# Performance work log

Hardware: AMD Instinct MI355X
Metric: run time of the kernel (lower is better)

The kernel has to match this reference:

```python
import jax, jax.numpy as jnp
import numpy as np

V = 512          # num vertices
F = 64           # pair-feature dim (gpnn_channels in)
C = 64           # gpnn_channels out
E = 8192         # num edges (avg degree 16)


def setup_inputs() -> dict:
    key = jax.random.key(0)
    k1, k2, k3, k4 = jax.random.split(key, 4)
    alpha = jax.random.normal(k1, (V * V, F), dtype=jnp.float32)          # pair features, row v*V+w
    edge_index = jax.random.randint(k2, (2, E), 0, V)                      # COO [src; dst]
    # GPNNEdgeConv.nn = MLP([F, C, C], act='relu')  (norm treated as identity / eval stats)
    w1 = jax.random.normal(k3, (F, C), dtype=jnp.float32) * (1.0 / np.sqrt(F))
    b1 = jnp.zeros((C,), dtype=jnp.float32)
    w2 = jax.random.normal(k4, (C, C), dtype=jnp.float32) * (1.0 / np.sqrt(C))
    b2 = jnp.zeros((C,), dtype=jnp.float32)
    eps = jnp.asarray(0.0, dtype=jnp.float32)                              # train_eps parameter
    return {"alpha": alpha, "edge_index": edge_index,
            "w1": w1, "b1": b1, "w2": w2, "b2": b2, "eps": eps}


def reference(alpha, edge_index, w1, b1, w2, b2, eps):
    # Dense 0/1 adjacency adj_t: adj[v, j] = 1 iff edge j -> v (dst-indexed, as spmm(adj_t, .)).
    adj = jnp.zeros((V, V), dtype=alpha.dtype).at[edge_index[1], edge_index[0]].set(1.0)
    a3 = alpha.reshape(V, V, F)  # a3[v, j] = alpha[v*V + j]
    # message_and_aggregate: out[v*V+w] = row v of spmm(adj_t, A_{v,w}),
    # where A_{v,w}[j] = alpha[v*V+j] + alpha[w*V+j]  (sum aggregation)
    #   = sum_j adj[v,j] * (a3[v,j] + a3[w,j]) = S[v] + T[v,w]
    S = jnp.einsum('vj,vjf->vf', adj, a3)    # [V, F]
    T = jnp.einsum('vj,wjf->vwf', adj, a3)   # [V, V, F]
    out = (S[:, None, :] + T).reshape(V * V, F)
    # GINConv residual: out + (1 + eps) * x_r, then MLP (Linear-ReLU-Linear)
    out = out + (1.0 + eps) * alpha
    h = jax.nn.relu(out @ w1 + b1)
    return h @ w2 + b2
```

## Files before the change

kernel.cpp:

```cpp
#include <hip/hip_runtime.h>
#include <hip/hip_bf16.h>

#define NV 512
#define NF 64

typedef __attribute__((ext_vector_type(8))) short bf16x8;
typedef __attribute__((ext_vector_type(4))) float f32x4;

union BF8 { bf16x8 v; unsigned u[4]; };

__device__ __forceinline__ unsigned short f2bf(float x) {
    unsigned u = __float_as_uint(x);
    unsigned r = (u + 0x7fffu + ((u >> 16) & 1u)) >> 16;
    return (unsigned short)r;
}

__device__ __forceinline__ unsigned awt_addr(int f, int jbyte) {
    return (unsigned)((f * 1024 + jbyte) ^ (((f ^ (f >> 3)) & 7) << 4));
}
__device__ __forceinline__ unsigned wt_addr(int m, int n, int kbyte) {
    return (unsigned)(m * 8192 + ((n * 128 + kbyte) ^ (((n ^ (n >> 3)) & 7) << 4)));
}

__global__ void k_zero(unsigned int* mask) {
    mask[blockIdx.x * 256 + threadIdx.x] = 0u;
}

__global__ void k_edges(const int* __restrict__ ei, int E, unsigned int* __restrict__ mask) {
    int e = blockIdx.x * 256 + threadIdx.x;
    if (e < E) {
        int s = ei[e];
        int d = ei[E + e];
        atomicOr(&mask[d * 16 + (s >> 5)], 1u << (s & 31));
    }
}

__global__ void k_S(const unsigned int* __restrict__ mask, const float* __restrict__ alpha,
                    float* __restrict__ S) {
    int v = blockIdx.x;
    int f = threadIdx.x;
    float acc = 0.f;
    for (int wd = 0; wd < 16; ++wd) {
        unsigned int bits = mask[v * 16 + wd];
        while (bits) {
            int b = __ffs(bits) - 1;
            bits &= bits - 1;
            int j = wd * 32 + b;
            acc += alpha[((size_t)v * NV + j) * NF + f];
        }
    }
    S[v * NF + f] = acc;
}

#define SCR_OFF 65536

__global__ __launch_bounds__(512, 4) void k_main(
    const float* __restrict__ alpha, const float* __restrict__ w1, const float* __restrict__ b1,
    const float* __restrict__ w2, const float* __restrict__ b2, const float* __restrict__ eps_p,
    const unsigned int* __restrict__ mask, const float* __restrict__ S,
    float* __restrict__ out)
{
    extern __shared__ char smem[];

    const int w    = blockIdx.x;
    const int t    = threadIdx.x;
    const int lane = t & 63;
    const int wid  = t >> 6;
    const int nlo  = lane & 15;
    const int g    = lane >> 4;

    {
        const float* src = alpha + (size_t)w * (NV * NF);
#pragma unroll
        for (int i = 0; i < 2; ++i) {
            int task = i * 512 + t;
            int jb = task >> 4;
            int fq = task & 15;
            unsigned ua[4][4];
#pragma unroll
            for (int h = 0; h < 4; ++h) {
                f32x4 r0 = *(const f32x4*)(src + (size_t)(jb * 8 + 2 * h) * NF + fq * 4);
                f32x4 r1 = *(const f32x4*)(src + (size_t)(jb * 8 + 2 * h + 1) * NF + fq * 4);
#pragma unroll
                for (int c = 0; c < 4; ++c)
                    ua[c][h] = (unsigned)f2bf(r0[c]) | ((unsigned)f2bf(r1[c]) << 16);
            }
#pragma unroll
            for (int c = 0; c < 4; ++c) {
                BF8 p;
                p.u[0] = ua[c][0]; p.u[1] = ua[c][1]; p.u[2] = ua[c][2]; p.u[3] = ua[c][3];
                *(bf16x8*)(smem + awt_addr(fq * 4 + c, jb * 16)) = p.v;
            }
        }
    }

    const int mbase = wid * 64;
    unsigned qm[4][4];
#pragma unroll
    for (int mi = 0; mi < 4; ++mi) {
        const uint4 q = *(const uint4*)(mask + (size_t)(mbase + mi * 16 + nlo) * 16 + g * 4);
        qm[mi][0] = q.x; qm[mi][1] = q.y; qm[mi][2] = q.z; qm[mi][3] = q.w;
    }

    __syncthreads();

    f32x4 acc[4][4];
#pragma unroll
    for (int mi = 0; mi < 4; ++mi)
#pragma unroll
        for (int nt = 0; nt < 4; ++nt)
            acc[mi][nt] = (f32x4){0.f, 0.f, 0.f, 0.f};

#pragma unroll
    for (int kq = 0; kq < 4; ++kq)
#pragma unroll
        for (int kr = 0; kr < 4; ++kr) {
            const int kk = kq * 4 + kr;
            const int srcl = kq * 16 + nlo;
            BF8 afr[4];
#pragma unroll
            for (int mi = 0; mi < 4; ++mi) {
                unsigned word = (unsigned)__shfl((int)qm[mi][kr], srcl);
                unsigned byteb = (word >> (g * 8)) & 0xFFu;
#pragma unroll
                for (int h = 0; h < 4; ++h) {
                    unsigned b0 = (byteb >> (2 * h)) & 1u;
                    unsigned b1 = (byteb >> (2 * h + 1)) & 1u;
                    afr[mi].u[h] = (b0 ? 0x3F80u : 0u) | (b1 ? 0x3F800000u : 0u);
                }
            }
#pragma unroll
            for (int nt = 0; nt < 4; ++nt) {
                bf16x8 bfr = *(const bf16x8*)(smem + awt_addr(nt * 16 + nlo, kk * 64 + g * 16));
#pragma unroll
                for (int mi = 0; mi < 4; ++mi)
                    acc[mi][nt] = __builtin_amdgcn_mfma_f32_16x16x32_bf16(afr[mi].v, bfr, acc[mi][nt], 0, 0, 0);
            }
        }

    __syncthreads();

    if (t < 256) {
        int m  = t >> 7;
        int sub = t & 127;
        int jb = sub >> 4;
        int fq = sub & 15;
        const float* wsrc = m ? w2 : w1;
        unsigned ua[4][4];
#pragma unroll
        for (int h = 0; h < 4; ++h) {
            f32x4 r0 = *(const f32x4*)(wsrc + (size_t)(jb * 8 + 2 * h) * NF + fq * 4);
            f32x4 r1 = *(const f32x4*)(wsrc + (size_t)(jb * 8 + 2 * h + 1) * NF + fq * 4);
#pragma unroll
            for (int c = 0; c < 4; ++c)
                ua[c][h] = (unsigned)f2bf(r0[c]) | ((unsigned)f2bf(r1[c]) << 16);
        }
#pragma unroll
        for (int c = 0; c < 4; ++c) {
            BF8 p;
            p.u[0] = ua[c][0]; p.u[1] = ua[c][1]; p.u[2] = ua[c][2]; p.u[3] = ua[c][3];
            *(bf16x8*)(smem + wt_addr(m, fq * 4 + c, jb * 16)) = p.v;
        }
    }
    float b1v[4], b2v[4];
#pragma unroll
    for (int nt = 0; nt < 4; ++nt) {
        b1v[nt] = b1[nt * 16 + nlo];
        b2v[nt] = b2[nt * 16 + nlo];
    }
    const float ceps = 1.0f + eps_p[0];

    __syncthreads();

    char* myscr = smem + SCR_OFF + wid * 2048;
#pragma unroll
    for (int mi = 0; mi < 4; ++mi) {
        int v0 = mbase + mi * 16;
#pragma unroll
        for (int nt = 0; nt < 4; ++nt) {
            int f = nt * 16 + nlo;
#pragma unroll
            for (int r = 0; r < 4; ++r) {
                int v = v0 + g * 4 + r;
                float pre = acc[mi][nt][r] + S[v * NF + f]
                          + ceps * alpha[((size_t)v * NV + w) * NF + f];
                int row = g * 4 + r;
                *(unsigned short*)(myscr + row * 128 + ((2 * f) ^ ((row & 7) << 4))) = f2bf(pre);
            }
        }

        bf16x8 a0 = *(const bf16x8*)(myscr + nlo * 128 + ((g * 16) ^ ((nlo & 7) << 4)));
        bf16x8 a1 = *(const bf16x8*)(myscr + nlo * 128 + ((g * 16 + 64) ^ ((nlo & 7) << 4)));
        f32x4 accm[4];
#pragma unroll
        for (int nt = 0; nt < 4; ++nt) {
            bf16x8 wf0 = *(const bf16x8*)(smem + wt_addr(0, nt * 16 + nlo, g * 16));
            bf16x8 wf1 = *(const bf16x8*)(smem + wt_addr(0, nt * 16 + nlo, 64 + g * 16));
            f32x4 z = {0.f, 0.f, 0.f, 0.f};
            z = __builtin_amdgcn_mfma_f32_16x16x32_bf16(a0, wf0, z, 0, 0, 0);
            z = __builtin_amdgcn_mfma_f32_16x16x32_bf16(a1, wf1, z, 0, 0, 0);
            accm[nt] = z;
        }

#pragma unroll
        for (int nt = 0; nt < 4; ++nt)
#pragma unroll
            for (int r = 0; r < 4; ++r) {
                float hv = accm[nt][r] + b1v[nt];
                hv = hv > 0.f ? hv : 0.f;
                int row = g * 4 + r;
                *(unsigned short*)(myscr + row * 128 + ((2 * (nt * 16 + nlo)) ^ ((row & 7) << 4))) = f2bf(hv);
            }

        bf16x8 h0 = *(const bf16x8*)(myscr + nlo * 128 + ((g * 16) ^ ((nlo & 7) << 4)));
        bf16x8 h1 = *(const bf16x8*)(myscr + nlo * 128 + ((g * 16 + 64) ^ ((nlo & 7) << 4)));
#pragma unroll
        for (int nt = 0; nt < 4; ++nt) {
            bf16x8 wf0 = *(const bf16x8*)(smem + wt_addr(1, nt * 16 + nlo, g * 16));
            bf16x8 wf1 = *(const bf16x8*)(smem + wt_addr(1, nt * 16 + nlo, 64 + g * 16));
            f32x4 z = {0.f, 0.f, 0.f, 0.f};
            z = __builtin_amdgcn_mfma_f32_16x16x32_bf16(h0, wf0, z, 0, 0, 0);
            z = __builtin_amdgcn_mfma_f32_16x16x32_bf16(h1, wf1, z, 0, 0, 0);
#pragma unroll
            for (int r = 0; r < 4; ++r) {
                int vv = v0 + g * 4 + r;
                out[((size_t)vv * NV + w) * NF + nt * 16 + nlo] = z[r] + b2v[nt];
            }
        }
    }
}

extern "C" void kernel_launch(void* const* d_in, const int* in_sizes, int n_in,
                              void* d_out, int out_size, void* d_ws, size_t ws_size,
                              hipStream_t stream) {
    const float* alpha = (const float*)d_in[0];
    const int*   ei    = (const int*)d_in[1];
    const float* w1    = (const float*)d_in[2];
    const float* b1    = (const float*)d_in[3];
    const float* w2    = (const float*)d_in[4];
    const float* b2    = (const float*)d_in[5];
    const float* eps   = (const float*)d_in[6];
    float* out = (float*)d_out;
    int E = in_sizes[1] / 2;

    unsigned int* mask = (unsigned int*)d_ws;
    float* S = (float*)d_ws + 8192;

    k_zero <<<32, 256, 0, stream>>>(mask);
    k_edges<<<(E + 255) / 256, 256, 0, stream>>>(ei, E, mask);
    k_S    <<<NV, 64, 0, stream>>>(mask, alpha, S);

    const int smem_bytes = 81920;
    hipFuncSetAttribute(reinterpret_cast<const void*>(k_main),
                        hipFuncAttributeMaxDynamicSharedMemorySize, smem_bytes);
    k_main <<<NV, 512, smem_bytes, stream>>>(alpha, w1, b1, w2, b2, eps, mask, S, out);
}
```

Before: 70.89 us.

## Overlap alpha staging with first half GEMM and parallelize S reduction

The main kernel now stages the first half of the alpha tile into shared memory, syncs, then issues loads for the second half while running MFMAs on the first half. This hides part of the global-load latency behind compute. Mask words are read directly from global/cache per k-step instead of being preloaded into registers and shuffled. k_S is widened to 256 threads, splitting mask words across four waves with two accumulators and a shared-memory reduction, to raise memory-level parallelism. The added per-iteration mask loads could cost latency in the GEMM loop.

```diff
diff --git a/kernel.cpp b/kernel.cpp
--- a/kernel.cpp
+++ b/kernel.cpp
@@ -37,19 +37,27 @@
 
 __global__ void k_S(const unsigned int* __restrict__ mask, const float* __restrict__ alpha,
                     float* __restrict__ S) {
+    __shared__ float red[4][64];
     int v = blockIdx.x;
-    int f = threadIdx.x;
-    float acc = 0.f;
-    for (int wd = 0; wd < 16; ++wd) {
-        unsigned int bits = mask[v * 16 + wd];
+    int lane = threadIdx.x & 63;
+    int g = threadIdx.x >> 6;
+    float a0 = 0.f, a1 = 0.f;
+    for (int wd = g * 4; wd < g * 4 + 4; ++wd) {
+        unsigned bits = mask[v * 16 + wd];
         while (bits) {
-            int b = __ffs(bits) - 1;
-            bits &= bits - 1;
-            int j = wd * 32 + b;
-            acc += alpha[((size_t)v * NV + j) * NF + f];
-        }
-    }
-    S[v * NF + f] = acc;
+            int b0 = __ffs(bits) - 1; bits &= bits - 1;
+            float x0 = alpha[((size_t)v * NV + wd * 32 + b0) * NF + lane];
+            if (bits) {
+                int b1 = __ffs(bits) - 1; bits &= bits - 1;
+                a1 += alpha[((size_t)v * NV + wd * 32 + b1) * NF + lane];
+            }
+            a0 += x0;
+        }
+    }
+    red[g][lane] = a0 + a1;
+    __syncthreads();
+    if (g == 0)
+        S[v * NF + lane] = red[0][lane] + red[1][lane] + red[2][lane] + red[3][lane];
 }
 
 #define SCR_OFF 65536
@@ -68,41 +76,29 @@
     const int wid  = t >> 6;
     const int nlo  = lane & 15;
     const int g    = lane >> 4;
-
-    {
-        const float* src = alpha + (size_t)w * (NV * NF);
-#pragma unroll
-        for (int i = 0; i < 2; ++i) {
-            int task = i * 512 + t;
-            int jb = task >> 4;
-            int fq = task & 15;
-            unsigned ua[4][4];
-#pragma unroll
-            for (int h = 0; h < 4; ++h) {
-                f32x4 r0 = *(const f32x4*)(src + (size_t)(jb * 8 + 2 * h) * NF + fq * 4);
-                f32x4 r1 = *(const f32x4*)(src + (size_t)(jb * 8 + 2 * h + 1) * NF + fq * 4);
-#pragma unroll
-                for (int c = 0; c < 4; ++c)
-                    ua[c][h] = (unsigned)f2bf(r0[c]) | ((unsigned)f2bf(r1[c]) << 16);
-            }
-#pragma unroll
-            for (int c = 0; c < 4; ++c) {
-                BF8 p;
-                p.u[0] = ua[c][0]; p.u[1] = ua[c][1]; p.u[2] = ua[c][2]; p.u[3] = ua[c][3];
-                *(bf16x8*)(smem + awt_addr(fq * 4 + c, jb * 16)) = p.v;
-            }
-        }
-    }
-
     const int mbase = wid * 64;
-    unsigned qm[4][4];
-#pragma unroll
-    for (int mi = 0; mi < 4; ++mi) {
-        const uint4 q = *(const uint4*)(mask + (size_t)(mbase + mi * 16 + nlo) * 16 + g * 4);
-        qm[mi][0] = q.x; qm[mi][1] = q.y; qm[mi][2] = q.z; qm[mi][3] = q.w;
-    }
-
-    __syncthreads();
+    const float* src = alpha + (size_t)w * (NV * NF);
+
+    auto stage_half = [&](int i) {
+        int task = i * 512 + t;
+        int jb = task >> 4;
+        int fq = task & 15;
+        unsigned ua[4][4];
+#pragma unroll
+        for (int h = 0; h < 4; ++h) {
+            f32x4 r0 = *(const f32x4*)(src + (size_t)(jb * 8 + 2 * h) * NF + fq * 4);
+            f32x4 r1 = *(const f32x4*)(src + (size_t)(jb * 8 + 2 * h + 1) * NF + fq * 4);
+#pragma unroll
+            for (int c = 0; c < 4; ++c)
+                ua[c][h] = (unsigned)f2bf(r0[c]) | ((unsigned)f2bf(r1[c]) << 16);
+        }
+#pragma unroll
+        for (int c = 0; c < 4; ++c) {
+            BF8 p;
+            p.u[0] = ua[c][0]; p.u[1] = ua[c][1]; p.u[2] = ua[c][2]; p.u[3] = ua[c][3];
+            *(bf16x8*)(smem + awt_addr(fq * 4 + c, jb * 16)) = p.v;
+        }
+    };
 
     f32x4 acc[4][4];
 #pragma unroll
@@ -111,17 +107,19 @@
         for (int nt = 0; nt < 4; ++nt)
             acc[mi][nt] = (f32x4){0.f, 0.f, 0.f, 0.f};
 
-#pragma unroll
-    for (int kq = 0; kq < 4; ++kq)
-#pragma unroll
-        for (int kr = 0; kr < 4; ++kr) {
-            const int kk = kq * 4 + kr;
-            const int srcl = kq * 16 + nlo;
+    const unsigned int* maskrow = mask + (size_t)(mbase + nlo) * 16;
+
+    auto gemm8 = [&](int K0) {
+#pragma unroll 2
+        for (int kx = 0; kx < 8; ++kx) {
+            const int kk = K0 + kx;
+            unsigned wv[4];
+#pragma unroll
+            for (int mi = 0; mi < 4; ++mi) wv[mi] = maskrow[mi * 256 + kk];
             BF8 afr[4];
 #pragma unroll
             for (int mi = 0; mi < 4; ++mi) {
-                unsigned word = (unsigned)__shfl((int)qm[mi][kr], srcl);
-                unsigned byteb = (word >> (g * 8)) & 0xFFu;
+                unsigned byteb = (wv[mi] >> (g * 8)) & 0xFFu;
 #pragma unroll
                 for (int h = 0; h < 4; ++h) {
                     unsigned b0 = (byteb >> (2 * h)) & 1u;
@@ -137,7 +135,14 @@
                     acc[mi][nt] = __builtin_amdgcn_mfma_f32_16x16x32_bf16(afr[mi].v, bfr, acc[mi][nt], 0, 0, 0);
             }
         }
-
+    };
+
+    stage_half(0);
+    __syncthreads();
+    stage_half(1);
+    gemm8(0);
+    __syncthreads();
+    gemm8(8);
     __syncthreads();
 
     if (t < 256) {
@@ -248,7 +253,7 @@
 
     k_zero <<<32, 256, 0, stream>>>(mask);
     k_edges<<<(E + 255) / 256, 256, 0, stream>>>(ei, E, mask);
-    k_S    <<<NV, 64, 0, stream>>>(mask, alpha, S);
+    k_S    <<<NV, 256, 0, stream>>>(mask, alpha, S);
 
     const int smem_bytes = 81920;
     hipFuncSetAttribute(reinterpret_cast<const void*>(k_main),
```

After: 71.35 us. No clear change (+0.7%).
